# Kernel optimization log

Hardware: AMD Instinct MI355X
Metric: run time of the kernel (lower is better)

## Reference

```python
import jax, jax.numpy as jnp
import numpy as np

N_NODES = 40000
N_EDGES = 640000
D_MODEL = 128
N_LAYERS = 2


def setup_inputs() -> dict:
    key = jax.random.key(0)
    k1, k2, k3 = jax.random.split(key, 3)
    x = jax.random.normal(k1, (N_NODES, D_MODEL), dtype=jnp.float32)
    # Glorot-ish scaled weights per layer
    W = jax.random.normal(k2, (N_LAYERS, D_MODEL, D_MODEL), dtype=jnp.float32) / np.sqrt(D_MODEL)
    b = jnp.zeros((N_LAYERS, D_MODEL), dtype=jnp.float32)
    edge_index = jax.random.randint(k3, (2, N_EDGES), 0, N_NODES, dtype=jnp.int64)
    return {"x": x, "W": W, "b": b, "edge_index": edge_index}


def reference(x, W, b, edge_index):
    """Stacked DGL-style GraphConv (norm='both') layers on a flattened batched graph.

    Per layer: h' = D_in^{-1/2} A D_out^{-1/2} (h W) + b
    implemented as gather(src) -> per-edge normalize -> segment_sum(dst).
    """
    src = edge_index[0]
    dst = edge_index[1]
    n = x.shape[0]
    ones = jnp.ones((src.shape[0],), dtype=x.dtype)
    deg_out = jax.ops.segment_sum(ones, src, num_segments=n)  # out-degree of src nodes
    deg_in = jax.ops.segment_sum(ones, dst, num_segments=n)   # in-degree of dst nodes
    # symmetric normalization per edge: 1/sqrt(d_out(u) * d_in(v)), clipped to avoid div0
    edge_norm = jax.lax.rsqrt(jnp.clip(deg_out[src] * deg_in[dst], 1.0, None))  # [E]

    h = x
    for l in range(W.shape[0]):
        m = h @ W[l]                                   # [N, d] dense transform
        msg = m[src] * edge_norm[:, None]              # [E, d] gather + scale
        h = jax.ops.segment_sum(msg, dst, num_segments=n) + b[l]  # [N, d] scatter-add
    return h
```

## Files before the change

### kernel.cpp

```cpp
#include <hip/hip_runtime.h>
#include <hip/hip_fp16.h>

#define D_MODEL 128
#define NREP 8
#define FC 32

__device__ __forceinline__ bool sniff_i64(const void* ei) {
    const long long* p64 = (const long long*)ei;
    bool f64 = true;
#pragma unroll
    for (int i = 0; i < 8; ++i) {
        long long v = p64[i];
        f64 = f64 && (v >= 0 && v < (1LL << 31));
    }
    return f64;
}

__device__ __forceinline__ void load_edge(const void* ei, int e, int nE, bool f64,
                                          int& s, int& d) {
    if (f64) {
        const long long* p64 = (const long long*)ei;
        s = (int)p64[e];
        d = (int)p64[(size_t)nE + e];
    } else {
        const int* p32 = (const int*)ei;
        s = p32[e];
        d = p32[(size_t)nE + e];
    }
}

__global__ __launch_bounds__(1024) void hist_kernel(const void* __restrict__ ei,
                                                    int* __restrict__ Cs,
                                                    int* __restrict__ Cd,
                                                    int nE, int n) {
    extern __shared__ int h[];
    bool f64 = sniff_i64(ei);
    int type = blockIdx.x & 1;
    int chunk = blockIdx.x >> 1;
    for (int i = threadIdx.x; i < n; i += 1024) h[i] = 0;
    __syncthreads();
    int ech = (nE + FC - 1) / FC;
    int e0 = chunk * ech;
    int e1 = min(nE, e0 + ech);
    size_t off = type ? (size_t)nE : 0;
    if (f64) {
        const long long* p64 = (const long long*)ei;
        for (int e = e0 + threadIdx.x; e < e1; e += 1024)
            atomicAdd(&h[(int)p64[off + e]], 1);
    } else {
        const int* p32 = (const int*)ei;
        for (int e = e0 + threadIdx.x; e < e1; e += 1024)
            atomicAdd(&h[p32[off + e]], 1);
    }
    __syncthreads();
    int* C = (type ? Cd : Cs) + (size_t)chunk * n;
    for (int i = threadIdx.x; i < n; i += 1024) C[i] = h[i];
}

__global__ void deg_reduce_kernel(const int* __restrict__ Cs,
                                  const int* __restrict__ Cd,
                                  float* __restrict__ a, float* __restrict__ bfac,
                                  float* __restrict__ ab, int* __restrict__ deg_in,
                                  int n) {
    int v = blockIdx.x * blockDim.x + threadIdx.x;
    if (v >= n) return;
    int dout = 0, din = 0;
#pragma unroll 8
    for (int c = 0; c < FC; ++c) {
        dout += Cs[(size_t)c * n + v];
        din += Cd[(size_t)c * n + v];
    }
    float fa = rsqrtf((float)max(dout, 1));
    float fb = rsqrtf((float)max(din, 1));
    a[v] = fa;
    bfac[v] = fb;
    ab[v] = fa * fb;
    deg_in[v] = din;
}

__global__ void prep_kernel(const void* __restrict__ ei, int* __restrict__ rep_out,
                            int* __restrict__ rep_in, int nE, int n) {
    bool f64 = sniff_i64(ei);
    int e = blockIdx.x * blockDim.x + threadIdx.x;
    if (e >= nE) return;
    int s, d;
    load_edge(ei, e, nE, f64, s, d);
    int rep = blockIdx.x & (NREP - 1);
    atomicAdd(&rep_out[(size_t)rep * n + s], 1);
    atomicAdd(&rep_in[(size_t)rep * n + d], 1);
}

__global__ void deg_reduce_rep_kernel(const int* __restrict__ rep_out,
                                      const int* __restrict__ rep_in,
                                      float* __restrict__ a, float* __restrict__ bfac,
                                      float* __restrict__ ab, int* __restrict__ deg_in,
                                      int n) {
    int v = blockIdx.x * blockDim.x + threadIdx.x;
    if (v >= n) return;
    int dout = 0, din = 0;
#pragma unroll
    for (int r = 0; r < NREP; ++r) {
        dout += rep_out[(size_t)r * n + v];
        din += rep_in[(size_t)r * n + v];
    }
    float fa = rsqrtf((float)max(dout, 1));
    float fb = rsqrtf((float)max(din, 1));
    a[v] = fa;
    bfac[v] = fb;
    ab[v] = fa * fb;
    deg_in[v] = din;
}

__global__ __launch_bounds__(1024) void scanA_kernel(const int* __restrict__ deg,
                                                     int* __restrict__ part, int n) {
    __shared__ int wsum[16];
    int i = blockIdx.x * 1024 + threadIdx.x;
    int lane = threadIdx.x & 63, wid = threadIdx.x >> 6;
    int v = (i < n) ? deg[i] : 0;
#pragma unroll
    for (int d = 32; d > 0; d >>= 1) v += __shfl_down(v, d, 64);
    if (lane == 0) wsum[wid] = v;
    __syncthreads();
    if (threadIdx.x == 0) {
        int s = 0;
#pragma unroll
        for (int w = 0; w < 16; ++w) s += wsum[w];
        part[blockIdx.x] = s;
    }
}

__global__ void scanB_kernel(const int* __restrict__ part, int* __restrict__ partx, int g) {
    if (blockIdx.x == 0 && threadIdx.x == 0) {
        int acc = 0;
        for (int i = 0; i < g; ++i) {
            partx[i] = acc;
            acc += part[i];
        }
    }
}

__global__ __launch_bounds__(1024) void scanC_kernel(const int* __restrict__ deg,
                                                     const int* __restrict__ partx,
                                                     int* __restrict__ offs, int n) {
    __shared__ int wsum[16];
    int i = blockIdx.x * 1024 + threadIdx.x;
    int lane = threadIdx.x & 63, wid = threadIdx.x >> 6;
    int v = (i < n) ? deg[i] : 0;
    int s = v;
#pragma unroll
    for (int d = 1; d < 64; d <<= 1) {
        int t = __shfl_up(s, d, 64);
        if (lane >= d) s += t;
    }
    if (lane == 63) wsum[wid] = s;
    __syncthreads();
    if (wid == 0) {
        int wsv = (lane < 16) ? wsum[lane] : 0;
#pragma unroll
        for (int d = 1; d < 16; d <<= 1) {
            int t = __shfl_up(wsv, d, 16);
            if ((lane & 15) >= d) wsv += t;
        }
        if (lane < 16) wsum[lane] = wsv;
    }
    __syncthreads();
    int base = partx[blockIdx.x] + ((wid > 0) ? wsum[wid - 1] : 0);
    int incl = base + s;
    if (i < n) {
        offs[i] = incl - v;
        if (i == n - 1) offs[n] = incl;
    }
}

__global__ void base_kernel(const int* __restrict__ Cd, const int* __restrict__ offs,
                            int* __restrict__ base, int n) {
    int v = blockIdx.x * blockDim.x + threadIdx.x;
    if (v >= n) return;
    int run = offs[v];
#pragma unroll 8
    for (int c = 0; c < FC; ++c) {
        base[(size_t)c * n + v] = run;
        run += Cd[(size_t)c * n + v];
    }
}

__global__ __launch_bounds__(1024) void fill_lds_kernel(const void* __restrict__ ei,
                                                        const int* __restrict__ base,
                                                        int* __restrict__ csr_src,
                                                        int nE, int n) {
    extern __shared__ int cur[];
    bool f64 = sniff_i64(ei);
    int chunk = blockIdx.x;
    for (int i = threadIdx.x; i < n; i += 1024) cur[i] = base[(size_t)chunk * n + i];
    __syncthreads();
    int ech = (nE + FC - 1) / FC;
    int e0 = chunk * ech;
    int e1 = min(nE, e0 + ech);
    for (int e = e0 + threadIdx.x; e < e1; e += 1024) {
        int s, d;
        load_edge(ei, e, nE, f64, s, d);
        int slot = atomicAdd(&cur[d], 1);
        csr_src[slot] = s;
    }
}

__global__ void fill_kernel(const void* __restrict__ ei, const int* __restrict__ offs,
                            int* __restrict__ cursor, int* __restrict__ csr_src, int nE) {
    bool f64 = sniff_i64(ei);
    int e = blockIdx.x * blockDim.x + threadIdx.x;
    if (e >= nE) return;
    int s, d;
    load_edge(ei, e, nE, f64, s, d);
    int slot = offs[d] + atomicAdd(&cursor[d], 1);
    csr_src[slot] = s;
}

__global__ void xcvt_kernel(const float* __restrict__ x, const float* __restrict__ a,
                            float2* __restrict__ xh, int n4) {
    int idx = blockIdx.x * blockDim.x + threadIdx.x;
    if (idx >= n4) return;
    int row = idx >> 5;
    float s = a[row];
    float4 v = ((const float4*)x)[idx];
    union { __half2 h2[2]; float2 f2; } u;
    u.h2[0] = __floats2half2_rn(s * v.x, s * v.y);
    u.h2[1] = __floats2half2_rn(s * v.z, s * v.w);
    xh[idx] = u.f2;
}

template <int MODE>
__global__ __launch_bounds__(256) void agg_kernel(const __half2* __restrict__ rows_in,
                                                  const int* __restrict__ offs,
                                                  const int* __restrict__ csr,
                                                  const float* __restrict__ ab,
                                                  const float* __restrict__ bfac,
                                                  const float* __restrict__ a_arr,
                                                  __half2* __restrict__ out_rows,
                                                  float* __restrict__ c_out, int n) {
    int node = blockIdx.x * 4 + (threadIdx.x >> 6);
    if (node >= n) return;
    node = __builtin_amdgcn_readfirstlane(node);
    int lane = threadIdx.x & 63;
    int beg = offs[node], end = offs[node + 1];
    float ax0 = 0.f, ay0 = 0.f, ax1 = 0.f, ay1 = 0.f;
    float cs = 0.f;
    int e = beg;
    for (; e + 1 < end; e += 2) {
        int s0 = csr[e], s1 = csr[e + 1];
        __half2 v0 = rows_in[(size_t)s0 * 64 + lane];
        __half2 v1 = rows_in[(size_t)s1 * 64 + lane];
        float2 f0 = __half22float2(v0);
        float2 f1 = __half22float2(v1);
        ax0 += f0.x; ay0 += f0.y;
        ax1 += f1.x; ay1 += f1.y;
        if (MODE == 1) cs += a_arr[s0] + a_arr[s1];
    }
    if (e < end) {
        int s0 = csr[e];
        __half2 v0 = rows_in[(size_t)s0 * 64 + lane];
        float2 f0 = __half22float2(v0);
        ax0 += f0.x; ay0 += f0.y;
        if (MODE == 1) cs += a_arr[s0];
    }
    float sx = ax0 + ax1, sy = ay0 + ay1;
    if (MODE == 0) {
        float sc = ab[node];
        out_rows[(size_t)node * 64 + lane] = __floats2half2_rn(sc * sx, sc * sy);
    } else {
        out_rows[(size_t)node * 64 + lane] = __floats2half2_rn(sx, sy);
        if (lane == 0) c_out[node] = bfac[node] * cs;
    }
}

__global__ void wc_kernel(const float* __restrict__ W, const float* __restrict__ b,
                          float* __restrict__ wc) {
    int gid = blockIdx.x * blockDim.x + threadIdx.x;
    if (gid >= 129 * 128) return;
    int r = gid >> 7, j = gid & 127;
    const float* W2 = W + 128 * 128;
    float acc = 0.f;
    if (r < 128) {
        const float* w1r = W + (size_t)r * 128;
#pragma unroll 4
        for (int k = 0; k < 128; ++k) acc = fmaf(w1r[k], W2[(size_t)k * 128 + j], acc);
    } else {
#pragma unroll 4
        for (int k = 0; k < 128; ++k) acc = fmaf(b[k], W2[(size_t)k * 128 + j], acc);
    }
    wc[gid] = acc;
}

__global__ __launch_bounds__(256) void gemm_final_kernel(const __half2* __restrict__ A2,
                                                         const float* __restrict__ wc,
                                                         const float* __restrict__ bfac,
                                                         const float* __restrict__ c_arr,
                                                         const float* __restrict__ b2,
                                                         float* __restrict__ out, int nRows) {
    __shared__ float Ws[32][128];
    __shared__ float At[32][36];
    int tid = threadIdx.x;
    int tc = tid & 31;
    int tr = tid >> 5;
    int row0 = blockIdx.x * 32;
    float acc[4][4] = {};

    for (int k0 = 0; k0 < D_MODEL; k0 += 32) {
        __syncthreads();
        {
            const float4* Wg = (const float4*)(wc + (size_t)k0 * D_MODEL);
            float4* WsV = (float4*)&Ws[0][0];
#pragma unroll
            for (int i = 0; i < 4; ++i) WsV[tid + 256 * i] = Wg[tid + 256 * i];
        }
        int k0h = k0 >> 1;
#pragma unroll
        for (int i = 0; i < 2; ++i) {
            int lin = tid + 256 * i;
            int r = lin >> 4;
            int h = lin & 15;
            int row = row0 + r;
            __half2 v = (row < nRows) ? A2[(size_t)row * 64 + k0h + h]
                                      : __floats2half2_rn(0.f, 0.f);
            float2 f = __half22float2(v);
            At[2 * h][r] = f.x;
            At[2 * h + 1][r] = f.y;
        }
        __syncthreads();
#pragma unroll
        for (int kk = 0; kk < 32; ++kk) {
            float4 w4 = *(const float4*)&Ws[kk][4 * tc];
            float4 a4 = *(const float4*)&At[kk][4 * tr];
            float wv[4] = {w4.x, w4.y, w4.z, w4.w};
            float av[4] = {a4.x, a4.y, a4.z, a4.w};
#pragma unroll
            for (int i = 0; i < 4; ++i)
#pragma unroll
                for (int j = 0; j < 4; ++j)
                    acc[i][j] = fmaf(av[i], wv[j], acc[i][j]);
        }
    }
    float4 g4 = *(const float4*)(wc + 128 * 128 + 4 * tc);
    float4 b4 = *(const float4*)(b2 + 4 * tc);
#pragma unroll
    for (int i = 0; i < 4; ++i) {
        int row = row0 + 4 * tr + i;
        if (row < nRows) {
            float bf = bfac[row];
            float cv = c_arr[row];
            float4 o;
            o.x = bf * acc[i][0] + cv * g4.x + b4.x;
            o.y = bf * acc[i][1] + cv * g4.y + b4.y;
            o.z = bf * acc[i][2] + cv * g4.z + b4.z;
            o.w = bf * acc[i][3] + cv * g4.w + b4.w;
            *(float4*)(out + (size_t)row * D_MODEL + 4 * tc) = o;
        }
    }
}

extern "C" void kernel_launch(void* const* d_in, const int* in_sizes, int n_in,
                              void* d_out, int out_size, void* d_ws, size_t ws_size,
                              hipStream_t stream) {
    const float* x = (const float*)d_in[0];
    const float* W = (const float*)d_in[1];
    const float* b = (const float*)d_in[2];
    const void* ei = d_in[3];
    const int D = D_MODEL;
    int N = in_sizes[0] / D;
    int E = in_sizes[3] / 2;
    float* out = (float*)d_out;

    char* p = (char*)d_ws;
    size_t off = 0;
    auto take = [&](size_t bytes) {
        void* r = p + off;
        off += (bytes + 255) & ~(size_t)255;
        return r;
    };
    __half2* xh   = (__half2*)take((size_t)N * D * 2);
    __half2* u    = (__half2*)take((size_t)N * D * 2);
    int* csr_src  = (int*)take((size_t)E * 4);
    float* a_arr  = (float*)take((size_t)N * 4);
    float* bfac   = (float*)take((size_t)N * 4);
    float* ab     = (float*)take((size_t)N * 4);
    float* c_arr  = (float*)take((size_t)N * 4);
    int* deg_in   = (int*)take((size_t)N * 4);
    int* offs     = (int*)take((size_t)(N + 1) * 4);
    int* cursor   = (int*)take((size_t)N * 4);
    int* part     = (int*)take(256 * 4);
    int* partx    = (int*)take(256 * 4);
    float* wc     = (float*)take((size_t)129 * 128 * 4);
    size_t common = off;
    int* Cs   = (int*)take((size_t)FC * N * 4);
    int* Cd   = (int*)take((size_t)FC * N * 4);
    int* base = (int*)take((size_t)FC * N * 4);
    size_t lds_need = off;
    __half2* t2 = xh;

    size_t lds_bytes = (size_t)N * 4;
    bool use_lds = (lds_bytes <= 160000) && (lds_need <= ws_size);

    int eb = (E + 255) / 256;
    int G = (N + 1023) / 1024;

    wc_kernel<<<(129 * 128 + 255) / 256, 256, 0, stream>>>(W, b, wc);

    if (use_lds) {
        hist_kernel<<<2 * FC, 1024, lds_bytes, stream>>>(ei, Cs, Cd, E, N);
        deg_reduce_kernel<<<(N + 255) / 256, 256, 0, stream>>>(Cs, Cd, a_arr, bfac,
                                                               ab, deg_in, N);
        scanA_kernel<<<G, 1024, 0, stream>>>(deg_in, part, N);
        scanB_kernel<<<1, 64, 0, stream>>>(part, partx, G);
        scanC_kernel<<<G, 1024, 0, stream>>>(deg_in, partx, offs, N);
        base_kernel<<<(N + 255) / 256, 256, 0, stream>>>(Cd, offs, base, N);
        fill_lds_kernel<<<FC, 1024, lds_bytes, stream>>>(ei, base, csr_src, E, N);
    } else {
        int* rep_out = (int*)Cs;
        int* rep_in  = (int*)Cd;
        if (lds_need > ws_size) {
            rep_out = (int*)u;
            rep_in  = (int*)((char*)u + (size_t)NREP * N * 4);
        }
        hipMemsetAsync(rep_out, 0, (size_t)NREP * N * 4, stream);
        hipMemsetAsync(rep_in, 0, (size_t)NREP * N * 4, stream);
        hipMemsetAsync(cursor, 0, (size_t)N * 4, stream);
        prep_kernel<<<eb, 256, 0, stream>>>(ei, rep_out, rep_in, E, N);
        deg_reduce_rep_kernel<<<(N + 255) / 256, 256, 0, stream>>>(rep_out, rep_in, a_arr,
                                                                   bfac, ab, deg_in, N);
        scanA_kernel<<<G, 1024, 0, stream>>>(deg_in, part, N);
        scanB_kernel<<<1, 64, 0, stream>>>(part, partx, G);
        scanC_kernel<<<G, 1024, 0, stream>>>(deg_in, partx, offs, N);
        fill_kernel<<<eb, 256, 0, stream>>>(ei, offs, cursor, csr_src, E);
    }

    int n4 = N * (D / 4);
    xcvt_kernel<<<(n4 + 255) / 256, 256, 0, stream>>>(x, a_arr, (float2*)xh, n4);

    agg_kernel<0><<<(N + 3) / 4, 256, 0, stream>>>(xh, offs, csr_src, ab, bfac, a_arr,
                                                   u, c_arr, N);
    agg_kernel<1><<<(N + 3) / 4, 256, 0, stream>>>(u, offs, csr_src, ab, bfac, a_arr,
                                                   t2, c_arr, N);
    gemm_final_kernel<<<(N + 31) / 32, 256, 0, stream>>>(t2, wc, bfac, c_arr,
                                                         b + 128, out, N);
}
```

Baseline: 159.8 us.

## Pack src/dst histograms into one word and fuse degree/scan/base kernels

```diff
diff --git a/kernel.cpp b/kernel.cpp
--- a/kernel.cpp
+++ b/kernel.cpp
@@ -30,52 +30,141 @@
 }
 
 __global__ __launch_bounds__(1024) void hist_kernel(const void* __restrict__ ei,
-                                                    int* __restrict__ Cs,
-                                                    int* __restrict__ Cd,
+                                                    unsigned int* __restrict__ Cpk,
                                                     int nE, int n) {
-    extern __shared__ int h[];
+    extern __shared__ unsigned int h[];
     bool f64 = sniff_i64(ei);
-    int type = blockIdx.x & 1;
-    int chunk = blockIdx.x >> 1;
+    int chunk = blockIdx.x;
     for (int i = threadIdx.x; i < n; i += 1024) h[i] = 0;
     __syncthreads();
     int ech = (nE + FC - 1) / FC;
     int e0 = chunk * ech;
     int e1 = min(nE, e0 + ech);
-    size_t off = type ? (size_t)nE : 0;
     if (f64) {
         const long long* p64 = (const long long*)ei;
-        for (int e = e0 + threadIdx.x; e < e1; e += 1024)
-            atomicAdd(&h[(int)p64[off + e]], 1);
+        for (int e = e0 + threadIdx.x; e < e1; e += 1024) {
+            atomicAdd(&h[(int)p64[e]], 1u);
+            atomicAdd(&h[(int)p64[(size_t)nE + e]], 0x10000u);
+        }
     } else {
         const int* p32 = (const int*)ei;
-        for (int e = e0 + threadIdx.x; e < e1; e += 1024)
-            atomicAdd(&h[p32[off + e]], 1);
-    }
-    __syncthreads();
-    int* C = (type ? Cd : Cs) + (size_t)chunk * n;
+        for (int e = e0 + threadIdx.x; e < e1; e += 1024) {
+            atomicAdd(&h[p32[e]], 1u);
+            atomicAdd(&h[p32[(size_t)nE + e]], 0x10000u);
+        }
+    }
+    __syncthreads();
+    unsigned int* C = Cpk + (size_t)chunk * n;
     for (int i = threadIdx.x; i < n; i += 1024) C[i] = h[i];
 }
 
-__global__ void deg_reduce_kernel(const int* __restrict__ Cs,
-                                  const int* __restrict__ Cd,
-                                  float* __restrict__ a, float* __restrict__ bfac,
-                                  float* __restrict__ ab, int* __restrict__ deg_in,
-                                  int n) {
-    int v = blockIdx.x * blockDim.x + threadIdx.x;
-    if (v >= n) return;
-    int dout = 0, din = 0;
+__global__ __launch_bounds__(1024) void scanA_kernel(const unsigned int* __restrict__ Cpk,
+                                                     float* __restrict__ a,
+                                                     float* __restrict__ bfac,
+                                                     float* __restrict__ ab,
+                                                     int* __restrict__ deg_in,
+                                                     int* __restrict__ part, int n) {
+    __shared__ int wsum[16];
+    int i = blockIdx.x * 1024 + threadIdx.x;
+    int lane = threadIdx.x & 63, wid = threadIdx.x >> 6;
+    int din = 0;
+    if (i < n) {
+        int dout = 0;
 #pragma unroll 8
-    for (int c = 0; c < FC; ++c) {
-        dout += Cs[(size_t)c * n + v];
-        din += Cd[(size_t)c * n + v];
-    }
-    float fa = rsqrtf((float)max(dout, 1));
-    float fb = rsqrtf((float)max(din, 1));
-    a[v] = fa;
-    bfac[v] = fb;
-    ab[v] = fa * fb;
-    deg_in[v] = din;
+        for (int c = 0; c < FC; ++c) {
+            unsigned int w = Cpk[(size_t)c * n + i];
+            dout += (int)(w & 0xFFFFu);
+            din += (int)(w >> 16);
+        }
+        float fa = rsqrtf((float)max(dout, 1));
+        float fb = rsqrtf((float)max(din, 1));
+        a[i] = fa;
+        bfac[i] = fb;
+        ab[i] = fa * fb;
+        deg_in[i] = din;
+    }
+    int v = din;
+#pragma unroll
+    for (int d = 32; d > 0; d >>= 1) v += __shfl_down(v, d, 64);
+    if (lane == 0) wsum[wid] = v;
+    __syncthreads();
+    if (threadIdx.x == 0) {
+        int s = 0;
+#pragma unroll
+        for (int w = 0; w < 16; ++w) s += wsum[w];
+        part[blockIdx.x] = s;
+    }
+}
+
+__global__ void scanB_kernel(const int* __restrict__ part, int* __restrict__ partx, int g) {
+    if (blockIdx.x == 0 && threadIdx.x == 0) {
+        int acc = 0;
+        for (int i = 0; i < g; ++i) {
+            partx[i] = acc;
+            acc += part[i];
+        }
+    }
+}
+
+__global__ __launch_bounds__(1024) void scanC_kernel(const int* __restrict__ deg,
+                                                     const int* __restrict__ partx,
+                                                     const unsigned int* __restrict__ Cpk,
+                                                     int* __restrict__ offs,
+                                                     int* __restrict__ base, int n) {
+    __shared__ int wsum[16];
+    int i = blockIdx.x * 1024 + threadIdx.x;
+    int lane = threadIdx.x & 63, wid = threadIdx.x >> 6;
+    int v = (i < n) ? deg[i] : 0;
+    int s = v;
+#pragma unroll
+    for (int d = 1; d < 64; d <<= 1) {
+        int t = __shfl_up(s, d, 64);
+        if (lane >= d) s += t;
+    }
+    if (lane == 63) wsum[wid] = s;
+    __syncthreads();
+    if (wid == 0) {
+        int wsv = (lane < 16) ? wsum[lane] : 0;
+#pragma unroll
+        for (int d = 1; d < 16; d <<= 1) {
+            int t = __shfl_up(wsv, d, 16);
+            if ((lane & 15) >= d) wsv += t;
+        }
+        if (lane < 16) wsum[lane] = wsv;
+    }
+    __syncthreads();
+    int pfx = partx[blockIdx.x] + ((wid > 0) ? wsum[wid - 1] : 0);
+    int incl = pfx + s;
+    if (i < n) {
+        int run = incl - v;
+        offs[i] = run;
+        if (i == n - 1) offs[n] = incl;
+#pragma unroll 8
+        for (int c = 0; c < FC; ++c) {
+            base[(size_t)c * n + i] = run;
+            run += (int)(Cpk[(size_t)c * n + i] >> 16);
+        }
+    }
+}
+
+__global__ __launch_bounds__(1024) void fill_lds_kernel(const void* __restrict__ ei,
+                                                        const int* __restrict__ base,
+                                                        int* __restrict__ csr_src,
+                                                        int nE, int n) {
+    extern __shared__ int cur[];
+    bool f64 = sniff_i64(ei);
+    int chunk = blockIdx.x;
+    for (int i = threadIdx.x; i < n; i += 1024) cur[i] = base[(size_t)chunk * n + i];
+    __syncthreads();
+    int ech = (nE + FC - 1) / FC;
+    int e0 = chunk * ech;
+    int e1 = min(nE, e0 + ech);
+    for (int e = e0 + threadIdx.x; e < e1; e += 1024) {
+        int s, d;
+        load_edge(ei, e, nE, f64, s, d);
+        int slot = atomicAdd(&cur[d], 1);
+        csr_src[slot] = s;
+    }
 }
 
 __global__ void prep_kernel(const void* __restrict__ ei, int* __restrict__ rep_out,
@@ -111,8 +200,8 @@
     deg_in[v] = din;
 }
 
-__global__ __launch_bounds__(1024) void scanA_kernel(const int* __restrict__ deg,
-                                                     int* __restrict__ part, int n) {
+__global__ __launch_bounds__(1024) void scanA_plain_kernel(const int* __restrict__ deg,
+                                                           int* __restrict__ part, int n) {
     __shared__ int wsum[16];
     int i = blockIdx.x * 1024 + threadIdx.x;
     int lane = threadIdx.x & 63, wid = threadIdx.x >> 6;
@@ -129,19 +218,9 @@
     }
 }
 
-__global__ void scanB_kernel(const int* __restrict__ part, int* __restrict__ partx, int g) {
-    if (blockIdx.x == 0 && threadIdx.x == 0) {
-        int acc = 0;
-        for (int i = 0; i < g; ++i) {
-            partx[i] = acc;
-            acc += part[i];
-        }
-    }
-}
-
-__global__ __launch_bounds__(1024) void scanC_kernel(const int* __restrict__ deg,
-                                                     const int* __restrict__ partx,
-                                                     int* __restrict__ offs, int n) {
+__global__ __launch_bounds__(1024) void scanC_plain_kernel(const int* __restrict__ deg,
+                                                           const int* __restrict__ partx,
+                                                           int* __restrict__ offs, int n) {
     __shared__ int wsum[16];
     int i = blockIdx.x * 1024 + threadIdx.x;
     int lane = threadIdx.x & 63, wid = threadIdx.x >> 6;
@@ -164,43 +243,11 @@
         if (lane < 16) wsum[lane] = wsv;
     }
     __syncthreads();
-    int base = partx[blockIdx.x] + ((wid > 0) ? wsum[wid - 1] : 0);
-    int incl = base + s;
+    int pfx = partx[blockIdx.x] + ((wid > 0) ? wsum[wid - 1] : 0);
+    int incl = pfx + s;
     if (i < n) {
         offs[i] = incl - v;
         if (i == n - 1) offs[n] = incl;
-    }
-}
-
-__global__ void base_kernel(const int* __restrict__ Cd, const int* __restrict__ offs,
-                            int* __restrict__ base, int n) {
-    int v = blockIdx.x * blockDim.x + threadIdx.x;
-    if (v >= n) return;
-    int run = offs[v];
-#pragma unroll 8
-    for (int c = 0; c < FC; ++c) {
-        base[(size_t)c * n + v] = run;
-        run += Cd[(size_t)c * n + v];
-    }
-}
-
-__global__ __launch_bounds__(1024) void fill_lds_kernel(const void* __restrict__ ei,
-                                                        const int* __restrict__ base,
-                                                        int* __restrict__ csr_src,
-                                                        int nE, int n) {
-    extern __shared__ int cur[];
-    bool f64 = sniff_i64(ei);
-    int chunk = blockIdx.x;
-    for (int i = threadIdx.x; i < n; i += 1024) cur[i] = base[(size_t)chunk * n + i];
-    __syncthreads();
-    int ech = (nE + FC - 1) / FC;
-    int e0 = chunk * ech;
-    int e1 = min(nE, e0 + ech);
-    for (int e = e0 + threadIdx.x; e < e1; e += 1024) {
-        int s, d;
-        load_edge(ei, e, nE, f64, s, d);
-        int slot = atomicAdd(&cur[d], 1);
-        csr_src[slot] = s;
     }
 }
 
@@ -243,26 +290,34 @@
     int lane = threadIdx.x & 63;
     int beg = offs[node], end = offs[node + 1];
     float ax0 = 0.f, ay0 = 0.f, ax1 = 0.f, ay1 = 0.f;
+    float ax2 = 0.f, ay2 = 0.f, ax3 = 0.f, ay3 = 0.f;
     float cs = 0.f;
     int e = beg;
-    for (; e + 1 < end; e += 2) {
-        int s0 = csr[e], s1 = csr[e + 1];
+    for (; e + 3 < end; e += 4) {
+        int s0 = csr[e], s1 = csr[e + 1], s2 = csr[e + 2], s3 = csr[e + 3];
         __half2 v0 = rows_in[(size_t)s0 * 64 + lane];
         __half2 v1 = rows_in[(size_t)s1 * 64 + lane];
+        __half2 v2 = rows_in[(size_t)s2 * 64 + lane];
+        __half2 v3 = rows_in[(size_t)s3 * 64 + lane];
         float2 f0 = __half22float2(v0);
         float2 f1 = __half22float2(v1);
+        float2 f2 = __half22float2(v2);
+        float2 f3 = __half22float2(v3);
         ax0 += f0.x; ay0 += f0.y;
         ax1 += f1.x; ay1 += f1.y;
-        if (MODE == 1) cs += a_arr[s0] + a_arr[s1];
-    }
-    if (e < end) {
+        ax2 += f2.x; ay2 += f2.y;
+        ax3 += f3.x; ay3 += f3.y;
+        if (MODE == 1) cs += (a_arr[s0] + a_arr[s1]) + (a_arr[s2] + a_arr[s3]);
+    }
+    for (; e < end; ++e) {
         int s0 = csr[e];
         __half2 v0 = rows_in[(size_t)s0 * 64 + lane];
         float2 f0 = __half22float2(v0);
         ax0 += f0.x; ay0 += f0.y;
         if (MODE == 1) cs += a_arr[s0];
     }
-    float sx = ax0 + ax1, sy = ay0 + ay1;
+    float sx = (ax0 + ax1) + (ax2 + ax3);
+    float sy = (ay0 + ay1) + (ay2 + ay3);
     if (MODE == 0) {
         float sc = ab[node];
         out_rows[(size_t)node * 64 + lane] = __floats2half2_rn(sc * sx, sc * sy);
@@ -389,10 +444,8 @@
     int* part     = (int*)take(256 * 4);
     int* partx    = (int*)take(256 * 4);
     float* wc     = (float*)take((size_t)129 * 128 * 4);
-    size_t common = off;
-    int* Cs   = (int*)take((size_t)FC * N * 4);
-    int* Cd   = (int*)take((size_t)FC * N * 4);
-    int* base = (int*)take((size_t)FC * N * 4);
+    unsigned int* Cpk = (unsigned int*)take((size_t)FC * N * 4);
+    int* base     = (int*)take((size_t)FC * N * 4);
     size_t lds_need = off;
     __half2* t2 = xh;
 
@@ -405,17 +458,14 @@
     wc_kernel<<<(129 * 128 + 255) / 256, 256, 0, stream>>>(W, b, wc);
 
     if (use_lds) {
-        hist_kernel<<<2 * FC, 1024, lds_bytes, stream>>>(ei, Cs, Cd, E, N);
-        deg_reduce_kernel<<<(N + 255) / 256, 256, 0, stream>>>(Cs, Cd, a_arr, bfac,
-                                                               ab, deg_in, N);
-        scanA_kernel<<<G, 1024, 0, stream>>>(deg_in, part, N);
+        hist_kernel<<<FC, 1024, lds_bytes, stream>>>(ei, Cpk, E, N);
+        scanA_kernel<<<G, 1024, 0, stream>>>(Cpk, a_arr, bfac, ab, deg_in, part, N);
         scanB_kernel<<<1, 64, 0, stream>>>(part, partx, G);
-        scanC_kernel<<<G, 1024, 0, stream>>>(deg_in, partx, offs, N);
-        base_kernel<<<(N + 255) / 256, 256, 0, stream>>>(Cd, offs, base, N);
+        scanC_kernel<<<G, 1024, 0, stream>>>(deg_in, partx, Cpk, offs, base, N);
         fill_lds_kernel<<<FC, 1024, lds_bytes, stream>>>(ei, base, csr_src, E, N);
     } else {
-        int* rep_out = (int*)Cs;
-        int* rep_in  = (int*)Cd;
+        int* rep_out = (int*)Cpk;
+        int* rep_in  = (int*)base;
         if (lds_need > ws_size) {
             rep_out = (int*)u;
             rep_in  = (int*)((char*)u + (size_t)NREP * N * 4);
@@ -426,9 +476,9 @@
         prep_kernel<<<eb, 256, 0, stream>>>(ei, rep_out, rep_in, E, N);
         deg_reduce_rep_kernel<<<(N + 255) / 256, 256, 0, stream>>>(rep_out, rep_in, a_arr,
                                                                    bfac, ab, deg_in, N);
-        scanA_kernel<<<G, 1024, 0, stream>>>(deg_in, part, N);
+        scanA_plain_kernel<<<G, 1024, 0, stream>>>(deg_in, part, N);
         scanB_kernel<<<1, 64, 0, stream>>>(part, partx, G);
-        scanC_kernel<<<G, 1024, 0, stream>>>(deg_in, partx, offs, N);
+        scanC_plain_kernel<<<G, 1024, 0, stream>>>(deg_in, partx, offs, N);
         fill_kernel<<<eb, 256, 0, stream>>>(ei, offs, cursor, csr_src, E);
     }
 
```

After: 152.1 us. -4.8%, faster.
